# Performance work log

Measured on AMD Instinct MI355X. Metric: run time of the kernel, lower is better.

Reference implementation:

```python
import jax, jax.numpy as jnp
import numpy as np

B, N, IN_DIM, OUT_DIM, HEADS = 4, 2048, 128, 32, 8
NEG_SLOPE = 0.2


def setup_inputs() -> dict:
    key = jax.random.key(0)
    k_x, k_adj, k_w, k_as, k_ad = jax.random.split(key, 5)
    x = jax.random.normal(k_x, (B, N, IN_DIM), dtype=jnp.float32)
    adj = jax.random.randint(k_adj, (B, N, N), 0, 2).astype(jnp.float32)
    # xavier_uniform bounds
    lim_w = float(np.sqrt(6.0 / (IN_DIM + OUT_DIM)))
    lim_a = float(np.sqrt(6.0 / (OUT_DIM + 1)))
    W = jax.random.uniform(k_w, (HEADS, IN_DIM, OUT_DIM), dtype=jnp.float32, minval=-lim_w, maxval=lim_w)
    a_src = jax.random.uniform(k_as, (HEADS, OUT_DIM), dtype=jnp.float32, minval=-lim_a, maxval=lim_a)
    a_dst = jax.random.uniform(k_ad, (HEADS, OUT_DIM), dtype=jnp.float32, minval=-lim_a, maxval=lim_a)
    return {"x": x, "adj": adj, "W": W, "a_src": a_src, "a_dst": a_dst}


def reference(x, adj, W, a_src, a_dst):
    # Wh: [B,H,N,O]
    Wh = jnp.einsum('bnf,hfo->bhno', x, W)
    alpha_src = jnp.einsum('bhno,ho->bhn', Wh, a_src)  # [B,H,N]
    alpha_dst = jnp.einsum('bhno,ho->bhn', Wh, a_dst)  # [B,H,N]
    # additive scores e[b,h,i,j] = alpha_src[b,h,i] + alpha_dst[b,h,j]
    e = alpha_src[..., :, None] + alpha_dst[..., None, :]
    e = jnp.where(e >= 0, e, NEG_SLOPE * e)  # leaky_relu(0.2)
    n = adj.shape[-1]
    eye = jnp.eye(n, dtype=adj.dtype)
    mask = (adj + eye[None] > 0)[:, None, :, :]  # [B,1,N,N]
    e = jnp.where(mask, e, -jnp.inf)
    attn = jax.nn.softmax(e, axis=-1)  # every row has self-loop -> finite
    out = jnp.einsum('bhij,bhjo->bhio', attn, Wh)  # [B,H,N,O]
    b = x.shape[0]
    out = jnp.transpose(out, (0, 2, 1, 3)).reshape(b, n, HEADS * OUT_DIM)
    return jax.nn.relu(out)
```

## Files before the change

### kernel.cpp

```cpp
#include <hip/hip_runtime.h>
#include <math.h>

#define BB 4
#define NSZ 2048
#define FDIM 128
#define ODIM 32
#define HH 8

typedef short short8 __attribute__((ext_vector_type(8)));
typedef _Float16 half8 __attribute__((ext_vector_type(8)));
typedef float f32x4 __attribute__((ext_vector_type(4)));

#define WS_EAP  0
#define WS_EBP  131072
#define WS_ADJB 262144
#define WS_WHF  786432

__device__ __forceinline__ unsigned hpack(float a, float b) {
    unsigned r;
    asm("v_cvt_pkrtz_f16_f32 %0, %1, %2" : "=v"(r) : "v"(a), "v"(b));
    return r;
}

__global__ __launch_bounds__(256) void k_prep(const float* __restrict__ x,
                                              const float* __restrict__ adj,
                                              const float* __restrict__ W,
                                              const float* __restrict__ a_src,
                                              const float* __restrict__ a_dst,
                                              unsigned* __restrict__ adjb,
                                              int4* __restrict__ whf,
                                              float* __restrict__ eap,
                                              unsigned short* __restrict__ ebe,
                                              unsigned short* __restrict__ ebe2) {
    __shared__ float wsl[FDIM * 33];
    __shared__ unsigned short wlds[64][33];
    int t = threadIdx.x;

    if (blockIdx.x >= 1024) {
        int bid = blockIdx.x - 1024;
#pragma unroll
        for (int it = 0; it < 4; it++) {
            int g = (it * 4096 + bid) * 256 + t;
            int l = g & 7;
            int word = g >> 3;
            int wk = word & 63;
            int row = word >> 6;
            int i = row & (NSZ - 1);
            const float4 v = *(const float4*)&adj[(size_t)row * NSZ + wk * 32 + l * 4];
            unsigned m = 0;
            if (v.x > 0.f) m |= 1u << (l * 4 + 0);
            if (v.y > 0.f) m |= 1u << (l * 4 + 1);
            if (v.z > 0.f) m |= 1u << (l * 4 + 2);
            if (v.w > 0.f) m |= 1u << (l * 4 + 3);
            m |= (unsigned)__shfl_xor((int)m, 1);
            m |= (unsigned)__shfl_xor((int)m, 2);
            m |= (unsigned)__shfl_xor((int)m, 4);
            if (l == 0) {
                int jb = i - wk * 32;
                if (jb >= 0 && jb < 32) m |= 1u << jb;
                adjb[word] = m;
            }
        }
        return;
    }

    int bidx = blockIdx.x;
    int b = bidx >> 8;
    int h = (bidx >> 5) & 7;
    int nt = bidx & 31;
    int n0 = nt * 64;
    int w = t >> 6, lane = t & 63;
    int col = lane & 15, quad = lane >> 4;

#pragma unroll
    for (int m = 0; m < 16; m++) {
        int idx = t + m * 256;
        wsl[(idx >> 5) * 33 + (idx & 31)] = W[(size_t)h * (FDIM * ODIM) + idx];
    }

    const float* xp = x + ((size_t)(b * NSZ) + n0 + w * 16 + col) * FDIM + quad * 8;
    int4 afr[4];
#pragma unroll
    for (int kt = 0; kt < 4; kt++) {
        float4 xa = *(const float4*)(xp + kt * 32);
        float4 xb = *(const float4*)(xp + kt * 32 + 4);
        afr[kt] = make_int4((int)hpack(xa.x, xa.y), (int)hpack(xa.z, xa.w),
                            (int)hpack(xb.x, xb.y), (int)hpack(xb.z, xb.w));
    }
    __syncthreads();

    f32x4 alo = {0.f, 0.f, 0.f, 0.f};
    f32x4 ahi = {0.f, 0.f, 0.f, 0.f};
#pragma unroll
    for (int kt = 0; kt < 4; kt++) {
        half8 a8 = __builtin_bit_cast(half8, afr[kt]);
#pragma unroll
        for (int ot = 0; ot < 2; ot++) {
            unsigned d[4];
#pragma unroll
            for (int jp = 0; jp < 4; jp++) {
                float lo = wsl[(kt * 32 + quad * 8 + 2 * jp) * 33 + ot * 16 + col];
                float hi = wsl[(kt * 32 + quad * 8 + 2 * jp + 1) * 33 + ot * 16 + col];
                d[jp] = hpack(lo, hi);
            }
            int4 bf = make_int4((int)d[0], (int)d[1], (int)d[2], (int)d[3]);
            if (ot == 0)
                alo = __builtin_amdgcn_mfma_f32_16x16x32_f16(a8,
                        __builtin_bit_cast(half8, bf), alo, 0, 0, 0);
            else
                ahi = __builtin_amdgcn_mfma_f32_16x16x32_f16(a8,
                        __builtin_bit_cast(half8, bf), ahi, 0, 0, 0);
        }
    }

    float as0 = a_src[h * ODIM + col], as1 = a_src[h * ODIM + 16 + col];
    float ad0 = a_dst[h * ODIM + col], ad1 = a_dst[h * ODIM + 16 + col];
#pragma unroll
    for (int r = 0; r < 4; r++) {
        float pa = alo[r] * as0 + ahi[r] * as1;
        float pb = alo[r] * ad0 + ahi[r] * ad1;
#pragma unroll
        for (int mk = 1; mk <= 8; mk <<= 1) {
            pa += __shfl_xor(pa, mk);
            pb += __shfl_xor(pb, mk);
        }
        if (col == 0) {
            size_t idx = (size_t)(b * HH + h) * NSZ + n0 + w * 16 + quad * 4 + r;
            eap[idx]  = __expf(-0.8f * pa);
            ebe[idx]  = (unsigned short)(hpack(__expf(pb - 2.f), 0.f) & 0xffffu);
            ebe2[idx] = (unsigned short)(hpack(__expf(0.2f * pb - 2.f), 0.f) & 0xffffu);
        }
    }

#pragma unroll
    for (int r = 0; r < 4; r++) {
        wlds[w * 16 + quad * 4 + r][col]      = (unsigned short)(hpack(alo[r], 0.f) & 0xffffu);
        wlds[w * 16 + quad * 4 + r][col + 16] = (unsigned short)(hpack(ahi[r], 0.f) & 0xffffu);
    }
    __syncthreads();
    int jl = w >> 1, ot = w & 1;
    unsigned d[4];
#pragma unroll
    for (int jp = 0; jp < 4; jp++) {
        unsigned lo = wlds[jl * 32 + quad * 8 + 2 * jp][ot * 16 + col];
        unsigned hi = wlds[jl * 32 + quad * 8 + 2 * jp + 1][ot * 16 + col];
        d[jp] = (hi << 16) | lo;
    }
    int fragid = ((b * HH + h) * 64 + nt * 2 + jl) * 2 + ot;
    whf[(size_t)fragid * 64 + lane] = make_int4((int)d[0], (int)d[1], (int)d[2], (int)d[3]);
}

__device__ __forceinline__ int4 pfrag16(unsigned R2, uint4 e, uint4 g,
                                        unsigned w8,
                                        const unsigned (*__restrict__ mlut)[2]) {
    unsigned r0, r1, r2, r3, q0, q1, q2, q3;
    asm("v_pk_mul_f16 %0, %1, %2" : "=v"(r0) : "v"(R2), "v"(g.x));
    asm("v_pk_mul_f16 %0, %1, %2" : "=v"(r1) : "v"(R2), "v"(g.y));
    asm("v_pk_mul_f16 %0, %1, %2" : "=v"(r2) : "v"(R2), "v"(g.z));
    asm("v_pk_mul_f16 %0, %1, %2" : "=v"(r3) : "v"(R2), "v"(g.w));
    asm("v_pk_max_f16 %0, %1, %2" : "=v"(q0) : "v"(e.x), "v"(r0));
    asm("v_pk_max_f16 %0, %1, %2" : "=v"(q1) : "v"(e.y), "v"(r1));
    asm("v_pk_max_f16 %0, %1, %2" : "=v"(q2) : "v"(e.z), "v"(r2));
    asm("v_pk_max_f16 %0, %1, %2" : "=v"(q3) : "v"(e.w), "v"(r3));
    const unsigned* mA = mlut[w8 & 15];
    const unsigned* mB = mlut[(w8 >> 4) & 15];
    return make_int4((int)(q0 & mA[0]), (int)(q1 & mA[1]),
                     (int)(q2 & mB[0]), (int)(q3 & mB[1]));
}

__global__ __launch_bounds__(512, 4) void k_gat(const int4* __restrict__ whf,
                                                const float* __restrict__ eap,
                                                const unsigned short* __restrict__ ebe,
                                                const unsigned short* __restrict__ ebe2,
                                                const unsigned* __restrict__ adjb,
                                                float* __restrict__ out) {
    __shared__ __align__(16) float smem[6144];
    unsigned short* eble = (unsigned short*)smem;
    unsigned short* eblf = (unsigned short*)smem + 2048;
    unsigned (*mlut)[2] = (unsigned (*)[2])(smem + 2048);

    int t = threadIdx.x;
    int u = blockIdx.x;
    int unit = (u & 7) * 128 + (u >> 3);
    int b = unit >> 8;
    int h = (unit >> 5) & 7;
    int i0 = (unit & 31) * 64;
    int wave = t >> 6, lane = t & 63;
    int ih = wave >> 2, jq = wave & 3;
    int col = lane & 15, quad = lane >> 4, qsh = quad * 8;
    size_t bh = (size_t)(b * HH + h);

    if (t < 16) {
        mlut[t][0] = ((t & 1) ? 0x0000FFFFu : 0u) | ((t & 2) ? 0xFFFF0000u : 0u);
        mlut[t][1] = ((t & 4) ? 0x0000FFFFu : 0u) | ((t & 8) ? 0xFFFF0000u : 0u);
    }

    const float4* ege = (const float4*)(ebe + bh * NSZ);
    const float4* egf = (const float4*)(ebe2 + bh * NSZ);
    if (t < 256) ((float4*)eble)[t] = ege[t];
    else         ((float4*)eblf)[t - 256] = egf[t - 256];

    int iw = i0 + ih * 32;
    float Ra = eap[bh * NSZ + iw + col];
    float Rb = eap[bh * NSZ + iw + 16 + col];
    unsigned R20 = hpack(Ra, Ra);
    unsigned R21 = hpack(Rb, Rb);
    const char* mbase = (const char*)(adjb + ((size_t)(b * NSZ) + iw + col) * 64)
                        + (size_t)jq * 64;
    const int4* bfp = whf + bh * 8192 + (size_t)(jq * 16) * 128 + lane;

    f32x4 a00 = {0.f,0.f,0.f,0.f}, a01 = {0.f,0.f,0.f,0.f}, a0d = {0.f,0.f,0.f,0.f};
    f32x4 a10 = {0.f,0.f,0.f,0.f}, a11 = {0.f,0.f,0.f,0.f}, a1d = {0.f,0.f,0.f,0.f};
    const int4 onesv = make_int4(0x3C003C00, 0x3C003C00, 0x3C003C00, 0x3C003C00);
    half8 hones = __builtin_bit_cast(half8, onesv);

    __syncthreads();

    for (int g = 0; g < 4; g++) {
        uint4 m0 = *(const uint4*)(mbase + 0 * 4096 + g * 16);
        uint4 m1 = *(const uint4*)(mbase + 1 * 4096 + g * 16);
        int4 blo[4], bhi[4];
#pragma unroll
        for (int q = 0; q < 4; q++) {
            blo[q] = bfp[(g * 4 + q) * 128];
            bhi[q] = bfp[(g * 4 + q) * 128 + 64];
        }
        unsigned ma0[4] = {m0.x, m0.y, m0.z, m0.w};
        unsigned ma1[4] = {m1.x, m1.y, m1.z, m1.w};
#pragma unroll
        for (int q = 0; q < 4; q++) {
            int jt = jq * 16 + g * 4 + q;
            uint4 ef = *(const uint4*)&eble[jt * 32 + qsh];
            uint4 gf = *(const uint4*)&eblf[jt * 32 + qsh];
            half8 b0 = __builtin_bit_cast(half8, blo[q]);
            half8 b1 = __builtin_bit_cast(half8, bhi[q]);
            int4 f0 = pfrag16(R20, ef, gf, ma0[q] >> qsh, mlut);
            int4 f1 = pfrag16(R21, ef, gf, ma1[q] >> qsh, mlut);
            half8 af0 = __builtin_bit_cast(half8, f0);
            half8 af1 = __builtin_bit_cast(half8, f1);
            a00 = __builtin_amdgcn_mfma_f32_16x16x32_f16(af0, b0, a00, 0, 0, 0);
            a01 = __builtin_amdgcn_mfma_f32_16x16x32_f16(af0, b1, a01, 0, 0, 0);
            a0d = __builtin_amdgcn_mfma_f32_16x16x32_f16(af0, hones, a0d, 0, 0, 0);
            a10 = __builtin_amdgcn_mfma_f32_16x16x32_f16(af1, b0, a10, 0, 0, 0);
            a11 = __builtin_amdgcn_mfma_f32_16x16x32_f16(af1, b1, a11, 0, 0, 0);
            a1d = __builtin_amdgcn_mfma_f32_16x16x32_f16(af1, hones, a1d, 0, 0, 0);
        }
    }

    f32x4 (*cb)[3][64] = (f32x4 (*)[3][64])smem;
    __syncthreads();
    if (jq >= 2) {
        int s = ih * 4 + (jq - 2) * 2;
        cb[s][0][lane] = a00;  cb[s][1][lane] = a01;  cb[s][2][lane] = a0d;
        cb[s + 1][0][lane] = a10;  cb[s + 1][1][lane] = a11;  cb[s + 1][2][lane] = a1d;
    }
    __syncthreads();
    if (jq < 2) {
        int s = ih * 4 + jq * 2;
        a00 += cb[s][0][lane];  a01 += cb[s][1][lane];  a0d += cb[s][2][lane];
        a10 += cb[s + 1][0][lane];  a11 += cb[s + 1][1][lane];  a1d += cb[s + 1][2][lane];
    }
    __syncthreads();
    if (jq == 0) {
        int s = ih * 4;
        cb[s][0][lane] = a10;  cb[s][1][lane] = a11;  cb[s][2][lane] = a1d;
    } else if (jq == 1) {
        int s = ih * 4 + 1;
        cb[s][0][lane] = a00;  cb[s][1][lane] = a01;  cb[s][2][lane] = a0d;
    }
    __syncthreads();
    if (jq >= 2) return;
    f32x4 A0, A1, AD;
    if (jq == 0) {
        int s = ih * 4 + 1;
        A0 = a00 + cb[s][0][lane];
        A1 = a01 + cb[s][1][lane];
        AD = a0d + cb[s][2][lane];
    } else {
        int s = ih * 4;
        A0 = a10 + cb[s][0][lane];
        A1 = a11 + cb[s][1][lane];
        AD = a1d + cb[s][2][lane];
    }

    float* op = out + ((size_t)(b * NSZ) + iw + jq * 16) * (HH * ODIM) + h * ODIM + col;
#pragma unroll
    for (int r = 0; r < 4; r++) {
        int row = quad * 4 + r;
        float inv = 1.0f / AD[r];
        op[(size_t)row * (HH * ODIM)]      = fmaxf(A0[r] * inv, 0.f);
        op[(size_t)row * (HH * ODIM) + 16] = fmaxf(A1[r] * inv, 0.f);
    }
}

extern "C" void kernel_launch(void* const* d_in, const int* in_sizes, int n_in,
                              void* d_out, int out_size, void* d_ws, size_t ws_size,
                              hipStream_t stream) {
    const float* x     = (const float*)d_in[0];
    const float* adj   = (const float*)d_in[1];
    const float* W     = (const float*)d_in[2];
    const float* a_src = (const float*)d_in[3];
    const float* a_dst = (const float*)d_in[4];
    float* out = (float*)d_out;

    float* ws = (float*)d_ws;
    float* eap            = ws + WS_EAP;
    unsigned short* ebe   = (unsigned short*)(ws + WS_EBP);
    unsigned short* ebe2  = (unsigned short*)(ws + WS_EBP + 65536);
    unsigned* adjb        = (unsigned*)(ws + WS_ADJB);
    int4* whf             = (int4*)(ws + WS_WHF);

    k_prep<<<dim3(1024 + 4096), dim3(256), 0, stream>>>(x, adj, W, a_src, a_dst,
                                                        adjb, whf, eap, ebe, ebe2);
    k_gat<<<dim3(BB * HH * (NSZ / 64)), dim3(512), 0, stream>>>(whf, eap, ebe, ebe2, adjb, out);
}
```

Before: 129.3 us.

## Fuse prep and attention kernels into one cooperative kernel with grid sync

Replaces the two-kernel launch (prep, then GAT attention) with a single cooperative kernel of 512 persistent blocks. Each block first does projection and adjacency bit-packing work, then syncs the whole grid and processes two attention units. This removes the second launch and the gap between kernels, at the cost of a grid-wide barrier, fewer blocks in flight, and a host-side occupancy check before falling back to the old path.

```diff
diff --git a/kernel.cpp b/kernel.cpp
--- a/kernel.cpp
+++ b/kernel.cpp
@@ -1,5 +1,8 @@
 #include <hip/hip_runtime.h>
+#include <hip/hip_cooperative_groups.h>
 #include <math.h>
+
+namespace cg = cooperative_groups;
 
 #define BB 4
 #define NSZ 2048
@@ -7,7 +10,6 @@
 #define ODIM 32
 #define HH 8
 
-typedef short short8 __attribute__((ext_vector_type(8)));
 typedef _Float16 half8 __attribute__((ext_vector_type(8)));
 typedef float f32x4 __attribute__((ext_vector_type(4)));
 
@@ -20,6 +22,24 @@
     unsigned r;
     asm("v_cvt_pkrtz_f16_f32 %0, %1, %2" : "=v"(r) : "v"(a), "v"(b));
     return r;
+}
+
+__device__ __forceinline__ int4 pfrag16(unsigned R2, uint4 e, uint4 g,
+                                        unsigned w8,
+                                        const unsigned (*__restrict__ mlut)[2]) {
+    unsigned r0, r1, r2, r3, q0, q1, q2, q3;
+    asm("v_pk_mul_f16 %0, %1, %2" : "=v"(r0) : "v"(R2), "v"(g.x));
+    asm("v_pk_mul_f16 %0, %1, %2" : "=v"(r1) : "v"(R2), "v"(g.y));
+    asm("v_pk_mul_f16 %0, %1, %2" : "=v"(r2) : "v"(R2), "v"(g.z));
+    asm("v_pk_mul_f16 %0, %1, %2" : "=v"(r3) : "v"(R2), "v"(g.w));
+    asm("v_pk_max_f16 %0, %1, %2" : "=v"(q0) : "v"(e.x), "v"(r0));
+    asm("v_pk_max_f16 %0, %1, %2" : "=v"(q1) : "v"(e.y), "v"(r1));
+    asm("v_pk_max_f16 %0, %1, %2" : "=v"(q2) : "v"(e.z), "v"(r2));
+    asm("v_pk_max_f16 %0, %1, %2" : "=v"(q3) : "v"(e.w), "v"(r3));
+    const unsigned* mA = mlut[w8 & 15];
+    const unsigned* mB = mlut[(w8 >> 4) & 15];
+    return make_int4((int)(q0 & mA[0]), (int)(q1 & mA[1]),
+                     (int)(q2 & mB[0]), (int)(q3 & mB[1]));
 }
 
 __global__ __launch_bounds__(256) void k_prep(const float* __restrict__ x,
@@ -150,24 +170,6 @@
     whf[(size_t)fragid * 64 + lane] = make_int4((int)d[0], (int)d[1], (int)d[2], (int)d[3]);
 }
 
-__device__ __forceinline__ int4 pfrag16(unsigned R2, uint4 e, uint4 g,
-                                        unsigned w8,
-                                        const unsigned (*__restrict__ mlut)[2]) {
-    unsigned r0, r1, r2, r3, q0, q1, q2, q3;
-    asm("v_pk_mul_f16 %0, %1, %2" : "=v"(r0) : "v"(R2), "v"(g.x));
-    asm("v_pk_mul_f16 %0, %1, %2" : "=v"(r1) : "v"(R2), "v"(g.y));
-    asm("v_pk_mul_f16 %0, %1, %2" : "=v"(r2) : "v"(R2), "v"(g.z));
-    asm("v_pk_mul_f16 %0, %1, %2" : "=v"(r3) : "v"(R2), "v"(g.w));
-    asm("v_pk_max_f16 %0, %1, %2" : "=v"(q0) : "v"(e.x), "v"(r0));
-    asm("v_pk_max_f16 %0, %1, %2" : "=v"(q1) : "v"(e.y), "v"(r1));
-    asm("v_pk_max_f16 %0, %1, %2" : "=v"(q2) : "v"(e.z), "v"(r2));
-    asm("v_pk_max_f16 %0, %1, %2" : "=v"(q3) : "v"(e.w), "v"(r3));
-    const unsigned* mA = mlut[w8 & 15];
-    const unsigned* mB = mlut[(w8 >> 4) & 15];
-    return make_int4((int)(q0 & mA[0]), (int)(q1 & mA[1]),
-                     (int)(q2 & mB[0]), (int)(q3 & mB[1]));
-}
-
 __global__ __launch_bounds__(512, 4) void k_gat(const int4* __restrict__ whf,
                                                 const float* __restrict__ eap,
                                                 const unsigned short* __restrict__ ebe,
@@ -293,6 +295,263 @@
     }
 }
 
+__global__ __launch_bounds__(512, 4) void k_fused(
+        const float* __restrict__ x, const float* __restrict__ adj,
+        const float* __restrict__ W, const float* __restrict__ a_src,
+        const float* __restrict__ a_dst, unsigned* __restrict__ adjb,
+        int4* __restrict__ whf, float* __restrict__ eap,
+        unsigned short* __restrict__ ebe, unsigned short* __restrict__ ebe2,
+        float* __restrict__ out) {
+    __shared__ __align__(16) char smem[25600];
+    int t = threadIdx.x;
+    int blk = blockIdx.x;
+    int half = t >> 8, tt = t & 255;
+
+    {
+        float* wsl = (float*)smem;
+        unsigned short* wld = (unsigned short*)(smem + 16896) + half * 2112;
+
+        auto do_proj = [&]() {
+            int unit = blk * 2 + half;
+            int b = unit >> 8;
+            int h = (unit >> 5) & 7;
+            int nt = unit & 31;
+            int n0 = nt * 64;
+            int w = tt >> 6, lane = tt & 63;
+            int col = lane & 15, quad = lane >> 4;
+
+#pragma unroll
+            for (int m = 0; m < 8; m++) {
+                int idx = t + m * 512;
+                wsl[(idx >> 5) * 33 + (idx & 31)] = W[(size_t)h * (FDIM * ODIM) + idx];
+            }
+
+            const float* xp = x + ((size_t)(b * NSZ) + n0 + w * 16 + col) * FDIM + quad * 8;
+            int4 afr[4];
+#pragma unroll
+            for (int kt = 0; kt < 4; kt++) {
+                float4 xa = *(const float4*)(xp + kt * 32);
+                float4 xb = *(const float4*)(xp + kt * 32 + 4);
+                afr[kt] = make_int4((int)hpack(xa.x, xa.y), (int)hpack(xa.z, xa.w),
+                                    (int)hpack(xb.x, xb.y), (int)hpack(xb.z, xb.w));
+            }
+            __syncthreads();
+
+            f32x4 alo = {0.f, 0.f, 0.f, 0.f};
+            f32x4 ahi = {0.f, 0.f, 0.f, 0.f};
+#pragma unroll
+            for (int kt = 0; kt < 4; kt++) {
+                half8 a8 = __builtin_bit_cast(half8, afr[kt]);
+#pragma unroll
+                for (int ot = 0; ot < 2; ot++) {
+                    unsigned d[4];
+#pragma unroll
+                    for (int jp = 0; jp < 4; jp++) {
+                        float lo = wsl[(kt * 32 + quad * 8 + 2 * jp) * 33 + ot * 16 + col];
+                        float hi = wsl[(kt * 32 + quad * 8 + 2 * jp + 1) * 33 + ot * 16 + col];
+                        d[jp] = hpack(lo, hi);
+                    }
+                    int4 bf = make_int4((int)d[0], (int)d[1], (int)d[2], (int)d[3]);
+                    if (ot == 0)
+                        alo = __builtin_amdgcn_mfma_f32_16x16x32_f16(a8,
+                                __builtin_bit_cast(half8, bf), alo, 0, 0, 0);
+                    else
+                        ahi = __builtin_amdgcn_mfma_f32_16x16x32_f16(a8,
+                                __builtin_bit_cast(half8, bf), ahi, 0, 0, 0);
+                }
+            }
+
+            float as0 = a_src[h * ODIM + col], as1 = a_src[h * ODIM + 16 + col];
+            float ad0 = a_dst[h * ODIM + col], ad1 = a_dst[h * ODIM + 16 + col];
+#pragma unroll
+            for (int r = 0; r < 4; r++) {
+                float pa = alo[r] * as0 + ahi[r] * as1;
+                float pb = alo[r] * ad0 + ahi[r] * ad1;
+#pragma unroll
+                for (int mk = 1; mk <= 8; mk <<= 1) {
+                    pa += __shfl_xor(pa, mk);
+                    pb += __shfl_xor(pb, mk);
+                }
+                if (col == 0) {
+                    size_t idx = (size_t)(b * HH + h) * NSZ + n0 + w * 16 + quad * 4 + r;
+                    eap[idx]  = __expf(-0.8f * pa);
+                    ebe[idx]  = (unsigned short)(hpack(__expf(pb - 2.f), 0.f) & 0xffffu);
+                    ebe2[idx] = (unsigned short)(hpack(__expf(0.2f * pb - 2.f), 0.f) & 0xffffu);
+                }
+            }
+
+#pragma unroll
+            for (int r = 0; r < 4; r++) {
+                wld[(w * 16 + quad * 4 + r) * 33 + col]      = (unsigned short)(hpack(alo[r], 0.f) & 0xffffu);
+                wld[(w * 16 + quad * 4 + r) * 33 + col + 16] = (unsigned short)(hpack(ahi[r], 0.f) & 0xffffu);
+            }
+            __syncthreads();
+            int jl = w >> 1, ot = w & 1;
+            unsigned d[4];
+#pragma unroll
+            for (int jp = 0; jp < 4; jp++) {
+                unsigned lo = wld[(jl * 32 + quad * 8 + 2 * jp) * 33 + ot * 16 + col];
+                unsigned hi = wld[(jl * 32 + quad * 8 + 2 * jp + 1) * 33 + ot * 16 + col];
+                d[jp] = (hi << 16) | lo;
+            }
+            int fragid = ((b * HH + h) * 64 + nt * 2 + jl) * 2 + ot;
+            whf[(size_t)fragid * 64 + lane] = make_int4((int)d[0], (int)d[1], (int)d[2], (int)d[3]);
+        };
+
+        auto do_adj = [&]() {
+#pragma unroll 4
+            for (int it = 0; it < 16; it++) {
+                int g = (blk * 16 + it) * 512 + t;
+                int l = g & 7;
+                int word = g >> 3;
+                int wk = word & 63;
+                int row = word >> 6;
+                int i = row & (NSZ - 1);
+                const float4 v = *(const float4*)&adj[(size_t)row * NSZ + wk * 32 + l * 4];
+                unsigned m = 0;
+                if (v.x > 0.f) m |= 1u << (l * 4 + 0);
+                if (v.y > 0.f) m |= 1u << (l * 4 + 1);
+                if (v.z > 0.f) m |= 1u << (l * 4 + 2);
+                if (v.w > 0.f) m |= 1u << (l * 4 + 3);
+                m |= (unsigned)__shfl_xor((int)m, 1);
+                m |= (unsigned)__shfl_xor((int)m, 2);
+                m |= (unsigned)__shfl_xor((int)m, 4);
+                if (l == 0) {
+                    int jb = i - wk * 32;
+                    if (jb >= 0 && jb < 32) m |= 1u << jb;
+                    adjb[word] = m;
+                }
+            }
+        };
+
+        if (blk & 1) { do_proj(); do_adj(); }
+        else         { do_adj(); do_proj(); }
+    }
+
+    __threadfence();
+    cg::this_grid().sync();
+    __threadfence();
+
+    unsigned short* eble = (unsigned short*)smem;
+    unsigned short* eblf = (unsigned short*)smem + 2048;
+    f32x4 (*cb)[3][64] = (f32x4 (*)[3][64])smem;
+    unsigned (*mlut)[2] = (unsigned (*)[2])(smem + 24576);
+
+    int wave = t >> 6, lane = t & 63;
+    int ih = wave >> 2, jq = wave & 3;
+    int col = lane & 15, quad = lane >> 4, qsh = quad * 8;
+    const int4 onesv = make_int4(0x3C003C00, 0x3C003C00, 0x3C003C00, 0x3C003C00);
+    half8 hones = __builtin_bit_cast(half8, onesv);
+
+    if (t < 16) {
+        mlut[t][0] = ((t & 1) ? 0x0000FFFFu : 0u) | ((t & 2) ? 0xFFFF0000u : 0u);
+        mlut[t][1] = ((t & 4) ? 0x0000FFFFu : 0u) | ((t & 8) ? 0xFFFF0000u : 0u);
+    }
+
+    for (int rep = 0; rep < 2; rep++) {
+        __syncthreads();
+        int up = ((blk & 7) * 64 + (blk >> 3)) * 2 + rep;
+        int b = up >> 8;
+        int h = (up >> 5) & 7;
+        int i0 = (up & 31) * 64;
+        size_t bh = (size_t)(b * HH + h);
+
+        const float4* ege = (const float4*)(ebe + bh * NSZ);
+        const float4* egf = (const float4*)(ebe2 + bh * NSZ);
+        if (t < 256) ((float4*)eble)[t] = ege[t];
+        else         ((float4*)eblf)[t - 256] = egf[t - 256];
+
+        int iw = i0 + ih * 32;
+        float Ra = eap[bh * NSZ + iw + col];
+        float Rb = eap[bh * NSZ + iw + 16 + col];
+        unsigned R20 = hpack(Ra, Ra);
+        unsigned R21 = hpack(Rb, Rb);
+        const char* mbase = (const char*)(adjb + ((size_t)(b * NSZ) + iw + col) * 64)
+                            + (size_t)jq * 64;
+        const int4* bfp = (const int4*)whf + bh * 8192 + (size_t)(jq * 16) * 128 + lane;
+
+        f32x4 a00 = {0.f,0.f,0.f,0.f}, a01 = {0.f,0.f,0.f,0.f}, a0d = {0.f,0.f,0.f,0.f};
+        f32x4 a10 = {0.f,0.f,0.f,0.f}, a11 = {0.f,0.f,0.f,0.f}, a1d = {0.f,0.f,0.f,0.f};
+
+        __syncthreads();
+
+        for (int g = 0; g < 4; g++) {
+            uint4 m0 = *(const uint4*)(mbase + 0 * 4096 + g * 16);
+            uint4 m1 = *(const uint4*)(mbase + 1 * 4096 + g * 16);
+            int4 blo[4], bhi[4];
+#pragma unroll
+            for (int q = 0; q < 4; q++) {
+                blo[q] = bfp[(g * 4 + q) * 128];
+                bhi[q] = bfp[(g * 4 + q) * 128 + 64];
+            }
+            unsigned ma0[4] = {m0.x, m0.y, m0.z, m0.w};
+            unsigned ma1[4] = {m1.x, m1.y, m1.z, m1.w};
+#pragma unroll
+            for (int q = 0; q < 4; q++) {
+                int jt = jq * 16 + g * 4 + q;
+                uint4 ef = *(const uint4*)&eble[jt * 32 + qsh];
+                uint4 gf = *(const uint4*)&eblf[jt * 32 + qsh];
+                half8 b0 = __builtin_bit_cast(half8, blo[q]);
+                half8 b1 = __builtin_bit_cast(half8, bhi[q]);
+                int4 f0 = pfrag16(R20, ef, gf, ma0[q] >> qsh, mlut);
+                int4 f1 = pfrag16(R21, ef, gf, ma1[q] >> qsh, mlut);
+                half8 af0 = __builtin_bit_cast(half8, f0);
+                half8 af1 = __builtin_bit_cast(half8, f1);
+                a00 = __builtin_amdgcn_mfma_f32_16x16x32_f16(af0, b0, a00, 0, 0, 0);
+                a01 = __builtin_amdgcn_mfma_f32_16x16x32_f16(af0, b1, a01, 0, 0, 0);
+                a0d = __builtin_amdgcn_mfma_f32_16x16x32_f16(af0, hones, a0d, 0, 0, 0);
+                a10 = __builtin_amdgcn_mfma_f32_16x16x32_f16(af1, b0, a10, 0, 0, 0);
+                a11 = __builtin_amdgcn_mfma_f32_16x16x32_f16(af1, b1, a11, 0, 0, 0);
+                a1d = __builtin_amdgcn_mfma_f32_16x16x32_f16(af1, hones, a1d, 0, 0, 0);
+            }
+        }
+
+        __syncthreads();
+        if (jq >= 2) {
+            int s = ih * 4 + (jq - 2) * 2;
+            cb[s][0][lane] = a00;  cb[s][1][lane] = a01;  cb[s][2][lane] = a0d;
+            cb[s + 1][0][lane] = a10;  cb[s + 1][1][lane] = a11;  cb[s + 1][2][lane] = a1d;
+        }
+        __syncthreads();
+        if (jq < 2) {
+            int s = ih * 4 + jq * 2;
+            a00 += cb[s][0][lane];  a01 += cb[s][1][lane];  a0d += cb[s][2][lane];
+            a10 += cb[s + 1][0][lane];  a11 += cb[s + 1][1][lane];  a1d += cb[s + 1][2][lane];
+        }
+        __syncthreads();
+        if (jq == 0) {
+            int s = ih * 4;
+            cb[s][0][lane] = a10;  cb[s][1][lane] = a11;  cb[s][2][lane] = a1d;
+        } else if (jq == 1) {
+            int s = ih * 4 + 1;
+            cb[s][0][lane] = a00;  cb[s][1][lane] = a01;  cb[s][2][lane] = a0d;
+        }
+        __syncthreads();
+        if (jq < 2) {
+            f32x4 A0, A1, AD;
+            if (jq == 0) {
+                int s = ih * 4 + 1;
+                A0 = a00 + cb[s][0][lane];
+                A1 = a01 + cb[s][1][lane];
+                AD = a0d + cb[s][2][lane];
+            } else {
+                int s = ih * 4;
+                A0 = a10 + cb[s][0][lane];
+                A1 = a11 + cb[s][1][lane];
+                AD = a1d + cb[s][2][lane];
+            }
+            float* op = out + ((size_t)(b * NSZ) + iw + jq * 16) * (HH * ODIM) + h * ODIM + col;
+#pragma unroll
+            for (int r = 0; r < 4; r++) {
+                int row = quad * 4 + r;
+                float inv = 1.0f / AD[r];
+                op[(size_t)row * (HH * ODIM)]      = fmaxf(A0[r] * inv, 0.f);
+                op[(size_t)row * (HH * ODIM) + 16] = fmaxf(A1[r] * inv, 0.f);
+            }
+        }
+    }
+}
+
 extern "C" void kernel_launch(void* const* d_in, const int* in_sizes, int n_in,
                               void* d_out, int out_size, void* d_ws, size_t ws_size,
                               hipStream_t stream) {
@@ -310,6 +569,24 @@
     unsigned* adjb        = (unsigned*)(ws + WS_ADJB);
     int4* whf             = (int4*)(ws + WS_WHF);
 
+    static int coop_ok = -1;
+    if (coop_ok < 0) {
+        int nb = 0;
+        hipError_t qe = hipOccupancyMaxActiveBlocksPerMultiprocessor(
+            &nb, (const void*)k_fused, 512, 0);
+        coop_ok = (qe == hipSuccess && nb >= 2) ? 1 : 0;
+    }
+
+    if (coop_ok) {
+        void* args[] = {(void*)&x, (void*)&adj, (void*)&W, (void*)&a_src,
+                        (void*)&a_dst, (void*)&adjb, (void*)&whf, (void*)&eap,
+                        (void*)&ebe, (void*)&ebe2, (void*)&out};
+        hipError_t e = hipLaunchCooperativeKernel((const void*)k_fused, dim3(512),
+                                                  dim3(512), args, 0, stream);
+        if (e == hipSuccess) return;
+        coop_ok = 0;
+    }
+
     k_prep<<<dim3(1024 + 4096), dim3(256), 0, stream>>>(x, adj, W, a_src, a_dst,
                                                         adjb, whf, eap, ebe, ebe2);
     k_gat<<<dim3(BB * HH * (NSZ / 64)), dim3(512), 0, stream>>>(whf, eap, ebe, ebe2, adjb, out);
```

Result: no change. 129.3 us (+0.0%).
